# Kernel optimization log

Hardware: AMD Instinct MI355X
Metric: run time of the kernel (lower is better)

## Reference

```python
import jax, jax.numpy as jnp
import numpy as np

VOCAB = 256
D = 512
L = 2
FFN = 2048
H = 8
HD = D // H  # head dim = random-feature dim m for favor+
B = 2
T = 2048


def setup_inputs() -> dict:
    key = jax.random.key(0)
    ks = jax.random.split(key, 16)
    rng = np.random.default_rng(0)

    def lin(k, fan_in, shape):
        return jax.random.normal(k, shape, jnp.float32) / np.sqrt(fan_in)

    tokens = jax.random.randint(ks[0], (B, T), 0, VOCAB)
    emb = jax.random.normal(ks[1], (VOCAB, D // 2), jnp.float32)
    Wq = lin(ks[2], D, (L, D, D)); bq = 0.01 * jax.random.normal(ks[3], (L, D), jnp.float32)
    Wk = lin(ks[4], D, (L, D, D)); bk = 0.01 * jax.random.normal(ks[5], (L, D), jnp.float32)
    Wv = lin(ks[6], D, (L, D, D)); bv = 0.01 * jax.random.normal(ks[7], (L, D), jnp.float32)
    WU = lin(ks[8], D, (L, D, FFN)); bU = 0.01 * jax.random.normal(ks[9], (L, FFN), jnp.float32)
    WV = lin(ks[10], FFN, (L, FFN, D)); bV = 0.01 * jax.random.normal(ks[11], (L, D), jnp.float32)
    Wout = lin(ks[12], D, (D, VOCAB)); bout = 0.01 * jax.random.normal(ks[13], (VOCAB,), jnp.float32)
    ln1_g = jnp.ones((L, D), jnp.float32) + 0.02 * jax.random.normal(ks[14], (L, D), jnp.float32)
    ln2_g = jnp.ones((L, D), jnp.float32) + 0.02 * jax.random.normal(ks[15], (L, D), jnp.float32)
    ln1_b = jnp.zeros((L, D), jnp.float32)
    ln2_b = jnp.zeros((L, D), jnp.float32)
    # orthogonal random features per (layer, head), scaled by sqrt(head_dim)
    rfs_np = np.stack([
        np.stack([np.linalg.qr(rng.standard_normal((HD, HD)))[0] * np.sqrt(HD) for _ in range(H)])
        for _ in range(L)
    ]).astype(np.float32)
    rfs = jnp.asarray(rfs_np)
    return dict(tokens=tokens, emb=emb, Wq=Wq, bq=bq, Wk=Wk, bk=bk, Wv=Wv, bv=bv,
                rfs=rfs, ln1_g=ln1_g, ln1_b=ln1_b, ln2_g=ln2_g, ln2_b=ln2_b,
                WU=WU, bU=bU, WV=WV, bV=bV, Wout=Wout, bout=bout)


def _layernorm(x, g, b, eps=1e-5):
    mu = jnp.mean(x, -1, keepdims=True)
    var = jnp.mean((x - mu) ** 2, -1, keepdims=True)
    return (x - mu) * jax.lax.rsqrt(var + eps) * g + b


def _favor_feat(x, rfs):
    # x: [B,T,H,d]; rfs: [H,d,m]
    xp = x * (HD ** -0.25)
    return jnp.exp(jnp.einsum('bthd,hdm->bthm', xp, rfs)
                   - 0.5 * jnp.sum(xp ** 2, -1, keepdims=True))


def _attention(x, Wq, bq, Wk, bk, Wv, bv, rfs):
    Bx, Tx, Dm = x.shape
    q = (x @ Wq + bq).reshape(Bx, Tx, H, HD)
    k = (x @ Wk + bk).reshape(Bx, Tx, H, HD)
    v = (x @ Wv + bv).reshape(Bx, Tx, H, HD)
    qf = _favor_feat(q, rfs)  # [B,T,H,m]
    kf = _favor_feat(k, rfs)
    # causal prefix-sum (num_ps / den_ps with zero init sums)
    kv_cum = jnp.cumsum(jnp.einsum('bthm,bthd->bthmd', kf, v), axis=1)
    num = jnp.einsum('bthm,bthmd->bthd', qf, kv_cum)
    den = jnp.einsum('bthm,bthm->bth', qf, jnp.cumsum(kf, axis=1))
    return (num / (den[..., None] + 1e-16)).reshape(Bx, Tx, Dm)


def _pos_embs(x):
    # x: [B,T,D//2]; concat fixed sinusoidal embeddings of size D//2
    Bx, Tx, half = x.shape
    positions = jnp.arange(Tx, dtype=x.dtype)
    freqs = jnp.exp(jnp.arange(0, half, 2, dtype=x.dtype) * (-np.log(10000.0) / half))
    args = positions[:, None] * freqs[None, :]  # [T, half//2]
    sin = jnp.broadcast_to(jnp.sin(args)[None], (Bx, Tx, args.shape[1]))
    cos = jnp.broadcast_to(jnp.cos(args)[None], (Bx, Tx, args.shape[1]))
    return jnp.concatenate([x, sin, cos], -1)


def reference(tokens, emb, Wq, bq, Wk, bk, Wv, bv, rfs,
              ln1_g, ln1_b, ln2_g, ln2_b, WU, bU, WV, bV, Wout, bout):
    x = emb[tokens]            # [B,T,D//2]
    x = _pos_embs(x)           # [B,T,D]
    for i in range(L):
        skip = x
        a = _attention(x, Wq[i], bq[i], Wk[i], bk[i], Wv[i], bv[i], rfs[i])
        a = _layernorm(a, ln1_g[i], ln1_b[i])  # on_gptln=True: LN after attention
        x = skip + a
        skip = x
        h = jax.nn.gelu(x @ WU[i] + bU[i], approximate=False)
        h = h @ WV[i] + bV[i]
        h = _layernorm(h, ln2_g[i], ln2_b[i])  # on_gptln=True: LN after FFN
        x = skip + h
    return x @ Wout + bout     # [B,T,VOCAB]
```

## Files before the change

### kernel.cpp

```cpp
#include <hip/hip_runtime.h>
#include <hip/hip_bf16.h>
#include <math.h>

#define B_  2
#define T_  2048
#define D_  512
#define H_  8
#define HD_ 64
#define FFN_ 2048
#define VOCAB_ 256
#define BT_ (B_*T_)
#define NC_ 32
#define CENT_ 4160

typedef __attribute__((ext_vector_type(8))) short short8;
typedef __attribute__((ext_vector_type(4))) float float4v;
typedef __hip_bfloat16 bf16;

__device__ __forceinline__ void load16_lds(const void* g, void* l) {
  __builtin_amdgcn_global_load_lds(
      (const __attribute__((address_space(1))) unsigned int*)g,
      (__attribute__((address_space(3))) unsigned int*)l,
      16, 0, 0);
}

__global__ __launch_bounds__(512) void embed_pos_kernel(
    const int* __restrict__ tokens, const float* __restrict__ emb,
    float* __restrict__ x, bf16* __restrict__ xb)
{
  int bt = blockIdx.x;
  int t  = bt & (T_ - 1);
  int j  = threadIdx.x;
  float val;
  if (j < 256) {
    int tok = tokens[bt];
    val = emb[tok * 256 + j];
  } else {
    int jj = (j - 256) & 127;
    float f = expf(-(float)(2 * jj) * (9.210340371976184f / 256.0f));
    float arg = (float)t * f;
    val = (j < 384) ? sinf(arg) : cosf(arg);
  }
  size_t off = (size_t)bt * D_ + j;
  x[off]  = val;
  xb[off] = __float2bfloat16(val);
}

__global__ __launch_bounds__(256) void prep_all_kernel(
    const float* __restrict__ Wv, const float* __restrict__ WU,
    const float* __restrict__ WVp, const float* __restrict__ Wout,
    bf16* __restrict__ WvT, bf16* __restrict__ WUT,
    bf16* __restrict__ WVT, bf16* __restrict__ WoutT,
    const float* __restrict__ bq, const float* __restrict__ bk,
    const float* __restrict__ rfs, float* __restrict__ bqf,
    float* __restrict__ bkf)
{
  __shared__ float t[32][33];
  int id = blockIdx.x;
  if (id >= 4736) {
    int z = id - 4736;
    int l = z >> 1, side = z & 1;
    const float* b = (side ? bk : bq) + l * D_;
    float* bo = (side ? bkf : bqf) + l * D_;
    for (int n = threadIdx.x; n < D_; n += 256) {
      int h = n >> 6, j = n & 63;
      const float* R = rfs + ((size_t)l * H_ + h) * 4096;
      float acc = 0.f;
      for (int d = 0; d < 64; ++d) acc += b[h * 64 + d] * R[d * 64 + j];
      bo[n] = acc * 0.35355339059327373f;
    }
    return;
  }
  const float* W; bf16* Wt; int K, N, tx, ty;
  if (id < 512) {
    int l = id >> 8, tt = id & 255;
    W = Wv + (size_t)l * D_ * D_;  Wt = WvT + (size_t)l * D_ * D_;
    K = D_; N = D_; tx = tt & 15; ty = tt >> 4;
  } else if (id < 2560) {
    int tt = id - 512; int l = tt >> 10; tt &= 1023;
    W = WU + (size_t)l * D_ * FFN_;  Wt = WUT + (size_t)l * D_ * FFN_;
    K = D_; N = FFN_; tx = tt & 63; ty = tt >> 6;
  } else if (id < 4608) {
    int tt = id - 2560; int l = tt >> 10; tt &= 1023;
    W = WVp + (size_t)l * FFN_ * D_;  Wt = WVT + (size_t)l * FFN_ * D_;
    K = FFN_; N = D_; tx = tt & 15; ty = tt >> 4;
  } else {
    int tt = id - 4608;
    W = Wout;  Wt = WoutT;
    K = D_; N = VOCAB_; tx = tt & 7; ty = tt >> 3;
  }
  int n0 = tx * 32, k0 = ty * 32;
  int lx = threadIdx.x & 31, ly = threadIdx.x >> 5;
#pragma unroll
  for (int r = 0; r < 4; ++r)
    t[ly + 8 * r][lx] = W[(size_t)(k0 + ly + 8 * r) * N + n0 + lx];
  __syncthreads();
#pragma unroll
  for (int r = 0; r < 4; ++r)
    Wt[(size_t)(n0 + ly + 8 * r) * K + k0 + lx] = __float2bfloat16(t[lx][ly + 8 * r]);
}

__global__ __launch_bounds__(256) void rf_fold_w_kernel(
    const float* __restrict__ Wq, const float* __restrict__ Wk,
    const float* __restrict__ rfs, bf16* __restrict__ WqT, bf16* __restrict__ WkT)
{
  int h = blockIdx.x, kq = blockIdx.y, z = blockIdx.z;
  int l = z >> 1, side = z & 1;
  const float* W = (side ? Wk : Wq) + (size_t)l * D_ * D_;
  bf16* WT = (side ? WkT : WqT) + (size_t)l * D_ * D_;
  const float* Rg = rfs + ((size_t)l * H_ + h) * 4096;
  __shared__ float Rl[64][65];
  __shared__ float Ws[128][65];
  int tid = threadIdx.x;
  for (int i = tid; i < 1024; i += 256) {
    float4 v4 = ((const float4*)Rg)[i];
    int d = i >> 4, j0 = (i & 15) * 4;
    Rl[d][j0] = v4.x; Rl[d][j0+1] = v4.y; Rl[d][j0+2] = v4.z; Rl[d][j0+3] = v4.w;
  }
  for (int i = tid; i < 2048; i += 256) {
    int r = i >> 4, c0 = (i & 15) * 4;
    float4 v4 = *(const float4*)&W[(size_t)(kq * 128 + r) * D_ + h * 64 + c0];
    Ws[r][c0] = v4.x; Ws[r][c0+1] = v4.y; Ws[r][c0+2] = v4.z; Ws[r][c0+3] = v4.w;
  }
  __syncthreads();
  int lane = tid & 63, w = tid >> 6;
  for (int kh = 0; kh < 2; ++kh) {
    int kk = kh * 64 + lane;
#pragma unroll 1
    for (int jj = 0; jj < 16; ++jj) {
      int j = w * 16 + jj;
      float acc = 0.f;
#pragma unroll 16
      for (int d = 0; d < 64; ++d) acc += Ws[kk][d] * Rl[d][j];
      WT[(size_t)(h * 64 + j) * D_ + kq * 128 + kk] =
          __float2bfloat16(acc * 0.35355339059327373f);
    }
  }
}

__device__ __forceinline__ void mfma_core(
    const bf16* __restrict__ A, const bf16* __restrict__ Bt,
    int strideK, int kr, int row0, int col0, float4v acc[4][4])
{
  __shared__ short Al[128 * 64];
  __shared__ short Bl[128 * 64];
  int tid = threadIdx.x;
  int lane = tid & 63, w = tid >> 6;
  int wm = (w >> 1) * 64, wn = (w & 1) * 64;
  int quad = lane >> 4, l16 = lane & 15;

  int lr = lane >> 3;
  int ks = (((lane & 7) ^ lr)) * 8;
  const short* gA[4]; const short* gB[4];
  short* lA[4]; short* lB[4];
#pragma unroll
  for (int p = 0; p < 4; ++p) {
    int r = 32 * w + 8 * p;
    gA[p] = (const short*)A + (size_t)(row0 + r + lr) * strideK + ks;
    gB[p] = (const short*)Bt + (size_t)(col0 + r + lr) * strideK + ks;
    lA[p] = Al + r * 64;
    lB[p] = Bl + r * 64;
  }
#pragma unroll
  for (int p = 0; p < 4; ++p) {
    load16_lds(gA[p], lA[p]);
    load16_lds(gB[p], lB[p]);
  }

  for (int kt = 0; kt < kr; ++kt) {
    __syncthreads();
    short8 af[4][2], bfr[4][2];
#pragma unroll
    for (int mi = 0; mi < 4; ++mi) {
      int R = wm + mi * 16 + l16;
#pragma unroll
      for (int s = 0; s < 2; ++s) {
        int slot = (s * 4 + quad) ^ (R & 7);
        af[mi][s] = *(const short8*)&Al[R * 64 + slot * 8];
      }
    }
#pragma unroll
    for (int ni = 0; ni < 4; ++ni) {
      int R = wn + ni * 16 + l16;
#pragma unroll
      for (int s = 0; s < 2; ++s) {
        int slot = (s * 4 + quad) ^ (R & 7);
        bfr[ni][s] = *(const short8*)&Bl[R * 64 + slot * 8];
      }
    }
    __syncthreads();
    if (kt + 1 < kr) {
      int o = (kt + 1) * 64;
#pragma unroll
      for (int p = 0; p < 4; ++p) {
        load16_lds(gA[p] + o, lA[p]);
        load16_lds(gB[p] + o, lB[p]);
      }
    }
#pragma unroll
    for (int mi = 0; mi < 4; ++mi)
#pragma unroll
      for (int ni = 0; ni < 4; ++ni) {
        acc[mi][ni] = __builtin_amdgcn_mfma_f32_16x16x32_bf16(
            af[mi][0], bfr[ni][0], acc[mi][ni], 0, 0, 0);
        acc[mi][ni] = __builtin_amdgcn_mfma_f32_16x16x32_bf16(
            af[mi][1], bfr[ni][1], acc[mi][ni], 0, 0, 0);
      }
  }
}

__global__ __launch_bounds__(256) void gemm_mfma(
    const bf16* __restrict__ A, const bf16* __restrict__ Bt,
    const float* __restrict__ bias, void* __restrict__ Cout,
    int M, int N, int K, int mode)
{
  int lane = threadIdx.x & 63, w = threadIdx.x >> 6;
  int wm = (w >> 1) * 64, wn = (w & 1) * 64;
  int quad = lane >> 4, l16 = lane & 15;
  int row0 = blockIdx.y * 128, col0 = blockIdx.x * 128;
  float4v acc[4][4] = {};
  mfma_core(A, Bt, K, K >> 6, row0, col0, acc);
#pragma unroll
  for (int mi = 0; mi < 4; ++mi) {
#pragma unroll
    for (int ni = 0; ni < 4; ++ni) {
      int j = col0 + wn + ni * 16 + l16;
      float bj = bias[j];
#pragma unroll
      for (int r = 0; r < 4; ++r) {
        int i = row0 + wm + mi * 16 + quad * 4 + r;
        float v = acc[mi][ni][r] + bj;
        if (mode == 1) {
          v = 0.5f * v * (1.0f + erff(v * 0.7071067811865475f));
          ((bf16*)Cout)[(size_t)i * N + j] = __float2bfloat16(v);
        } else {
          ((float*)Cout)[(size_t)i * N + j] = v;
        }
      }
    }
  }
}

__global__ __launch_bounds__(256) void gemm_qkv(
    const bf16* __restrict__ A, const bf16* __restrict__ wT,
    const float* __restrict__ bqf, const float* __restrict__ bkf,
    const float* __restrict__ bv, float* __restrict__ outb, int l)
{
  int z = blockIdx.z;
  const bf16* Bt = wT + ((size_t)z * 2 + l) * D_ * D_;
  const float* bias = (z == 0 ? bqf : (z == 1 ? bkf : bv)) + l * D_;
  float* Cout = outb + (size_t)z * BT_ * D_;
  int lane = threadIdx.x & 63, w = threadIdx.x >> 6;
  int wm = (w >> 1) * 64, wn = (w & 1) * 64;
  int quad = lane >> 4, l16 = lane & 15;
  int row0 = blockIdx.y * 128, col0 = blockIdx.x * 128;
  float4v acc[4][4] = {};
  mfma_core(A, Bt, D_, D_ >> 6, row0, col0, acc);
  if (z < 2) {
#pragma unroll
    for (int mi = 0; mi < 4; ++mi) {
      float vres[4][4];
      float sq[4] = {0.f, 0.f, 0.f, 0.f};
#pragma unroll
      for (int ni = 0; ni < 4; ++ni) {
        int j = col0 + wn + ni * 16 + l16;
        float bj = bias[j];
#pragma unroll
        for (int r = 0; r < 4; ++r) {
          float v = acc[mi][ni][r] + bj;
          vres[ni][r] = v;
          sq[r] += v * v;
        }
      }
#pragma unroll
      for (int r = 0; r < 4; ++r) {
        float s = sq[r];
        s += __shfl_xor(s, 1, 64);
        s += __shfl_xor(s, 2, 64);
        s += __shfl_xor(s, 4, 64);
        s += __shfl_xor(s, 8, 64);
        sq[r] = s;
      }
#pragma unroll
      for (int ni = 0; ni < 4; ++ni) {
        int j = col0 + wn + ni * 16 + l16;
#pragma unroll
        for (int r = 0; r < 4; ++r) {
          int i = row0 + wm + mi * 16 + quad * 4 + r;
          Cout[(size_t)i * D_ + j] = __expf(vres[ni][r] - sq[r] * (1.0f / 128.0f));
        }
      }
    }
  } else {
#pragma unroll
    for (int mi = 0; mi < 4; ++mi) {
#pragma unroll
      for (int ni = 0; ni < 4; ++ni) {
        int j = col0 + wn + ni * 16 + l16;
        float bj = bias[j];
#pragma unroll
        for (int r = 0; r < 4; ++r) {
          int i = row0 + wm + mi * 16 + quad * 4 + r;
          Cout[(size_t)i * D_ + j] = acc[mi][ni][r] + bj;
        }
      }
    }
  }
}

__global__ __launch_bounds__(256) void gemm_splitk(
    const bf16* __restrict__ A, const bf16* __restrict__ Bt,
    float* __restrict__ P, int M, int N, int K, int KS)
{
  int s = blockIdx.z;
  int lane = threadIdx.x & 63, w = threadIdx.x >> 6;
  int wm = (w >> 1) * 64, wn = (w & 1) * 64;
  int quad = lane >> 4, l16 = lane & 15;
  int row0 = blockIdx.y * 128, col0 = blockIdx.x * 128;
  float4v acc[4][4] = {};
  mfma_core((const bf16*)((const short*)A + s * KS),
            (const bf16*)((const short*)Bt + s * KS),
            K, KS >> 6, row0, col0, acc);
  float* Ps = P + (size_t)s * M * N;
#pragma unroll
  for (int mi = 0; mi < 4; ++mi) {
#pragma unroll
    for (int ni = 0; ni < 4; ++ni) {
      int j = col0 + wn + ni * 16 + l16;
#pragma unroll
      for (int r = 0; r < 4; ++r) {
        int i = row0 + wm + mi * 16 + quad * 4 + r;
        Ps[(size_t)i * N + j] = acc[mi][ni][r];
      }
    }
  }
}

__global__ __launch_bounds__(256) void reduce4_bias_kernel(
    const float* __restrict__ P, const float* __restrict__ bias,
    float* __restrict__ C, int MN, int N)
{
  int idx = (blockIdx.x * 256 + threadIdx.x) * 4;
  float4 s0 = *(const float4*)&P[idx];
  float4 s1 = *(const float4*)&P[idx + MN];
  float4 s2 = *(const float4*)&P[idx + 2 * MN];
  float4 s3 = *(const float4*)&P[idx + 3 * MN];
  float4 b  = *(const float4*)&bias[idx & (N - 1)];
  float4 r;
  r.x = s0.x + s1.x + s2.x + s3.x + b.x;
  r.y = s0.y + s1.y + s2.y + s3.y + b.y;
  r.z = s0.z + s1.z + s2.z + s3.z + b.z;
  r.w = s0.w + s1.w + s2.w + s3.w + b.w;
  *(float4*)&C[idx] = r;
}

__global__ __launch_bounds__(256) void reduce_ln_add_kernel(
    const float* __restrict__ P, const float* __restrict__ bias,
    float* __restrict__ x, bf16* __restrict__ xb,
    const float* __restrict__ g, const float* __restrict__ bta)
{
  const int MN = BT_ * D_;
  int row = blockIdx.x;
  int tid = threadIdx.x;
  size_t base = (size_t)row * D_;
  float v0 = P[base + tid] + P[MN + base + tid] + P[2 * MN + base + tid]
           + P[3 * MN + base + tid] + bias[tid];
  float v1 = P[base + tid + 256] + P[MN + base + tid + 256]
           + P[2 * MN + base + tid + 256] + P[3 * MN + base + tid + 256]
           + bias[tid + 256];
  __shared__ float red[4];
  float w = v0 + v1;
  for (int o = 32; o > 0; o >>= 1) w += __shfl_down(w, o, 64);
  if ((tid & 63) == 0) red[tid >> 6] = w;
  __syncthreads();
  float mu = (red[0] + red[1] + red[2] + red[3]) * (1.f / 512.f);
  float d0 = v0 - mu, d1 = v1 - mu;
  __syncthreads();
  w = d0 * d0 + d1 * d1;
  for (int o = 32; o > 0; o >>= 1) w += __shfl_down(w, o, 64);
  if ((tid & 63) == 0) red[tid >> 6] = w;
  __syncthreads();
  float var = (red[0] + red[1] + red[2] + red[3]) * (1.f / 512.f);
  float rs = rsqrtf(var + 1e-5f);
  float n0 = x[base + tid]       + d0 * rs * g[tid]       + bta[tid];
  float n1 = x[base + tid + 256] + d1 * rs * g[tid + 256] + bta[tid + 256];
  x[base + tid]        = n0;
  x[base + tid + 256]  = n1;
  xb[base + tid]       = __float2bfloat16(n0);
  xb[base + tid + 256] = __float2bfloat16(n1);
}

__global__ __launch_bounds__(256) void chunk_sum_kernel(
    const float* __restrict__ kf, const float* __restrict__ v,
    float* __restrict__ buf)
{
  int bh = blockIdx.x / 31;
  int c  = blockIdx.x % 31;
  int b = bh >> 3, h = bh & 7;
  __shared__ float Ks[64][68], Vs[64][68];
  __shared__ float zpart[4][68];
  int tid = threadIdx.x;
  int d = tid & 63, g = tid >> 6;
  for (int t4 = 0; t4 < 64; t4 += 4) {
    int t = t4 + g;
    size_t off = ((size_t)(b * T_ + c * 64 + t) * D_) + h * 64 + d;
    Ks[t][d] = kf[off];
    Vs[t][d] = v[off];
  }
  __syncthreads();
  float acc[16];
#pragma unroll
  for (int i = 0; i < 16; ++i) acc[i] = 0.f;
  for (int t = 0; t < 64; ++t) {
    float vv = Vs[t][d];
#pragma unroll
    for (int i4 = 0; i4 < 4; ++i4) {
      float4 kv = *(const float4*)&Ks[t][g * 16 + i4 * 4];
      acc[i4*4+0] += kv.x * vv;
      acc[i4*4+1] += kv.y * vv;
      acc[i4*4+2] += kv.z * vv;
      acc[i4*4+3] += kv.w * vv;
    }
  }
  float zp = 0.f;
  for (int t = g * 16; t < g * 16 + 16; ++t) zp += Ks[t][d];
  zpart[g][d] = zp;
  size_t bo = (size_t)(bh * 31 + c) * CENT_;
#pragma unroll
  for (int i = 0; i < 16; ++i) buf[bo + (size_t)(g * 16 + i) * 64 + d] = acc[i];
  __syncthreads();
  if (tid < 64)
    buf[bo + 4096 + tid] = zpart[0][tid] + zpart[1][tid] + zpart[2][tid] + zpart[3][tid];
}

__global__ __launch_bounds__(256) void chunk_prefix_kernel(float* __restrict__ buf)
{
  int bh = blockIdx.x / 17;
  int grp = blockIdx.x % 17;
  int e = grp * 256 + threadIdx.x;
  if (e >= CENT_) return;
  size_t base = (size_t)bh * 31 * CENT_ + e;
  float vals[31];
#pragma unroll
  for (int c = 0; c < 31; ++c) vals[c] = buf[base + (size_t)c * CENT_];
  float run = 0.f;
#pragma unroll
  for (int c = 0; c < 31; ++c) {
    run += vals[c];
    buf[base + (size_t)c * CENT_] = run;
  }
}

__global__ __launch_bounds__(256) void chunk_attn_kernel(
    const float* __restrict__ qf, const float* __restrict__ kf,
    const float* __restrict__ v, const float* __restrict__ buf,
    float* __restrict__ out)
{
  int bh = blockIdx.x >> 5;
  int c  = blockIdx.x & 31;
  int b = bh >> 3, h = bh & 7;
  __shared__ float Qs[64][68], Ks[64][68], Vs[64][68];
  __shared__ float dpart[8][68];
  __shared__ float den[64];
  int tid = threadIdx.x;
  int d = tid & 63, g = tid >> 6;
  for (int t4 = 0; t4 < 64; t4 += 4) {
    int t = t4 + g;
    size_t off = ((size_t)(b * T_ + c * 64 + t) * D_) + h * 64 + d;
    Qs[t][d] = qf[off];
    Ks[t][d] = kf[off];
    Vs[t][d] = v[off];
  }
  __syncthreads();
  {
    int i = d;
    float a[16];
#pragma unroll
    for (int jj = 0; jj < 16; ++jj) a[jj] = 0.f;
    for (int m = 0; m < 64; m += 4) {
      float4 qv = *(const float4*)&Qs[i][m];
#pragma unroll
      for (int jj = 0; jj < 16; ++jj) {
        float4 kv = *(const float4*)&Ks[g * 16 + jj][m];
        a[jj] += qv.x * kv.x + qv.y * kv.y + qv.z * kv.z + qv.w * kv.w;
      }
    }
    __syncthreads();
    float rsum = 0.f;
#pragma unroll
    for (int jj = 0; jj < 16; ++jj) {
      int j = g * 16 + jj;
      a[jj] = (j <= i) ? a[jj] : 0.f;
      rsum += a[jj];
    }
#pragma unroll
    for (int j4 = 0; j4 < 4; ++j4)
      *(float4*)&Ks[i][g * 16 + j4 * 4] =
          make_float4(a[j4*4], a[j4*4+1], a[j4*4+2], a[j4*4+3]);
    dpart[g][i] = rsum;
  }
  const float* S0 = buf + (size_t)(bh * 31 + (c - 1)) * CENT_;
  {
    int i = d;
    float qz = 0.f;
    if (c > 0) {
      const float* z0 = S0 + 4096;
      for (int m = g * 16; m < g * 16 + 16; m += 4) {
        float4 qv = *(const float4*)&Qs[i][m];
        qz += qv.x * z0[m] + qv.y * z0[m+1] + qv.z * z0[m+2] + qv.w * z0[m+3];
      }
    }
    dpart[4 + g][i] = qz;
  }
  __syncthreads();
  if (tid < 64)
    den[tid] = dpart[0][tid] + dpart[1][tid] + dpart[2][tid] + dpart[3][tid]
             + dpart[4][tid] + dpart[5][tid] + dpart[6][tid] + dpart[7][tid];
  float acc[16];
#pragma unroll
  for (int ii = 0; ii < 16; ++ii) acc[ii] = 0.f;
  for (int j = 0; j < 64; j += 4) {
    float va = Vs[j][d], vb2 = Vs[j+1][d], vc = Vs[j+2][d], vd2 = Vs[j+3][d];
#pragma unroll
    for (int ii = 0; ii < 16; ++ii) {
      float4 av = *(const float4*)&Ks[g * 16 + ii][j];
      acc[ii] += av.x * va + av.y * vb2 + av.z * vc + av.w * vd2;
    }
  }
  if (c > 0) {
    for (int m = 0; m < 64; m += 4) {
      float sa = S0[(size_t)m * 64 + d];
      float sb2 = S0[(size_t)(m+1) * 64 + d];
      float sc = S0[(size_t)(m+2) * 64 + d];
      float sd2 = S0[(size_t)(m+3) * 64 + d];
#pragma unroll
      for (int ii = 0; ii < 16; ++ii) {
        float4 qv = *(const float4*)&Qs[g * 16 + ii][m];
        acc[ii] += qv.x * sa + qv.y * sb2 + qv.z * sc + qv.w * sd2;
      }
    }
  }
  __syncthreads();
#pragma unroll
  for (int ii = 0; ii < 16; ++ii) {
    int i = g * 16 + ii;
    size_t off = ((size_t)(b * T_ + c * 64 + i) * D_) + h * 64 + d;
    out[off] = acc[ii] / (den[i] + 1e-16f);
  }
}

__global__ __launch_bounds__(256) void ln_add_kernel(
    float* __restrict__ x, bf16* __restrict__ xb, const float* __restrict__ a,
    const float* __restrict__ g, const float* __restrict__ bta)
{
  int row = blockIdx.x;
  int tid = threadIdx.x;
  const float* ar = a + (size_t)row * D_;
  float v0 = ar[tid], v1 = ar[tid + 256];
  __shared__ float red[4];
  float w = v0 + v1;
  for (int o = 32; o > 0; o >>= 1) w += __shfl_down(w, o, 64);
  if ((tid & 63) == 0) red[tid >> 6] = w;
  __syncthreads();
  float mu = (red[0] + red[1] + red[2] + red[3]) * (1.f / 512.f);
  float d0 = v0 - mu, d1 = v1 - mu;
  __syncthreads();
  w = d0 * d0 + d1 * d1;
  for (int o = 32; o > 0; o >>= 1) w += __shfl_down(w, o, 64);
  if ((tid & 63) == 0) red[tid >> 6] = w;
  __syncthreads();
  float var = (red[0] + red[1] + red[2] + red[3]) * (1.f / 512.f);
  float rs = rsqrtf(var + 1e-5f);
  size_t xoff = (size_t)row * D_;
  float n0 = x[xoff + tid]       + d0 * rs * g[tid]       + bta[tid];
  float n1 = x[xoff + tid + 256] + d1 * rs * g[tid + 256] + bta[tid + 256];
  x[xoff + tid]        = n0;
  x[xoff + tid + 256]  = n1;
  xb[xoff + tid]       = __float2bfloat16(n0);
  xb[xoff + tid + 256] = __float2bfloat16(n1);
}

extern "C" void kernel_launch(void* const* d_in, const int* in_sizes, int n_in,
                              void* d_out, int out_size, void* d_ws, size_t ws_size,
                              hipStream_t stream) {
  const int*   tokens = (const int*)  d_in[0];
  const float* emb    = (const float*)d_in[1];
  const float* Wq     = (const float*)d_in[2];
  const float* bq     = (const float*)d_in[3];
  const float* Wk     = (const float*)d_in[4];
  const float* bk     = (const float*)d_in[5];
  const float* Wv     = (const float*)d_in[6];
  const float* bv     = (const float*)d_in[7];
  const float* rfs    = (const float*)d_in[8];
  const float* ln1g   = (const float*)d_in[9];
  const float* ln1b   = (const float*)d_in[10];
  const float* ln2g   = (const float*)d_in[11];
  const float* ln2b   = (const float*)d_in[12];
  const float* WU     = (const float*)d_in[13];
  const float* bU     = (const float*)d_in[14];
  const float* WV     = (const float*)d_in[15];
  const float* bV     = (const float*)d_in[16];
  const float* Wout   = (const float*)d_in[17];
  const float* bout   = (const float*)d_in[18];
  float* out = (float*)d_out;

  const size_t R = (size_t)BT_ * D_;
  float* ws = (float*)d_ws;
  float* x  = ws + 0 * R;
  float* ab = ws + 1 * R;
  float* qb = ws + 2 * R;
  float* kb = ws + 3 * R;
  float* vb = ws + 4 * R;
  float* sb = ws + 5 * R;
  bf16*  xb = (bf16*)(ws + 6 * R);
  bf16*  hb = (bf16*)qb;
  float* pb = ws + 16 * R;
  bf16* wT    = (bf16*)(ws + 6 * R + R / 2);
  bf16* WqT   = wT;
  bf16* WkT   = WqT + (size_t)2 * D_ * D_;
  bf16* WvT   = WkT + (size_t)2 * D_ * D_;
  bf16* WUT   = WvT + (size_t)2 * D_ * D_;
  bf16* WVT   = WUT + (size_t)2 * D_ * FFN_;
  bf16* WoutT = WVT + (size_t)2 * D_ * FFN_;
  float* bqf  = (float*)(WoutT + (size_t)VOCAB_ * D_);
  float* bkf  = bqf + 2 * D_;

  rf_fold_w_kernel<<<dim3(8, 4, 4), 256, 0, stream>>>(Wq, Wk, rfs, WqT, WkT);
  prep_all_kernel<<<4740, 256, 0, stream>>>(
      Wv, WU, WV, Wout, WvT, WUT, WVT, WoutT, bq, bk, rfs, bqf, bkf);

  embed_pos_kernel<<<BT_, 512, 0, stream>>>(tokens, emb, x, xb);

  for (int l = 0; l < 2; ++l) {
    gemm_qkv<<<dim3(D_/128, BT_/128, 3), 256, 0, stream>>>(
        xb, wT, bqf, bkf, bv, qb, l);

    chunk_sum_kernel<<<16 * 31, 256, 0, stream>>>(kb, vb, sb);
    chunk_prefix_kernel<<<16 * 17, 256, 0, stream>>>(sb);
    chunk_attn_kernel<<<16 * NC_, 256, 0, stream>>>(qb, kb, vb, sb, ab);

    ln_add_kernel<<<BT_, 256, 0, stream>>>(x, xb, ab, ln1g + l*D_, ln1b + l*D_);

    gemm_mfma<<<dim3(FFN_/128, BT_/128), 256, 0, stream>>>(
        xb, WUT + (size_t)l*D_*FFN_, bU + l*FFN_, hb, BT_, FFN_, D_, 1);

    gemm_splitk<<<dim3(D_/128, BT_/128, 4), 256, 0, stream>>>(
        hb, WVT + (size_t)l*FFN_*D_, pb, BT_, D_, FFN_, FFN_/4);
    reduce_ln_add_kernel<<<BT_, 256, 0, stream>>>(
        pb, bV + l*D_, x, xb, ln2g + l*D_, ln2b + l*D_);
  }

  gemm_splitk<<<dim3(VOCAB_/128, BT_/128, 4), 256, 0, stream>>>(
      xb, WoutT, pb, BT_, VOCAB_, D_, D_/4);
  reduce4_bias_kernel<<<(BT_*VOCAB_)/1024, 256, 0, stream>>>(
      pb, bout, out, BT_*VOCAB_, VOCAB_);
}
```

Baseline: 372.6 us.

## Store Q/K/V features in bf16 and use MFMA in chunked linear attention

The QKV GEMM now writes bf16 outputs instead of fp32, halving activation traffic. The chunk_sum and chunk_attn kernels are rewritten to stage bf16 tiles in swizzled LDS and compute K^T V, QK^T, A·V and Q·S0 with bf16 MFMA instructions instead of scalar FP32 FMAs. The workspace layout is reshuffled to fit the smaller buffers. This trades precision, since the random-feature values and the masked score matrix are rounded to bf16, for less memory traffic and matrix-core throughput in the attention stage.

```diff
diff --git a/kernel.cpp b/kernel.cpp
--- a/kernel.cpp
+++ b/kernel.cpp
@@ -22,6 +22,15 @@
       (const __attribute__((address_space(1))) unsigned int*)g,
       (__attribute__((address_space(3))) unsigned int*)l,
       16, 0, 0);
+}
+
+__device__ __forceinline__ unsigned short f2bf(float f) {
+  bf16 h = __float2bfloat16(f);
+  return __builtin_bit_cast(unsigned short, h);
+}
+__device__ __forceinline__ float bf2f(unsigned short u) {
+  unsigned int i = ((unsigned int)u) << 16;
+  return __builtin_bit_cast(float, i);
 }
 
 __global__ __launch_bounds__(512) void embed_pos_kernel(
@@ -244,12 +253,12 @@
 __global__ __launch_bounds__(256) void gemm_qkv(
     const bf16* __restrict__ A, const bf16* __restrict__ wT,
     const float* __restrict__ bqf, const float* __restrict__ bkf,
-    const float* __restrict__ bv, float* __restrict__ outb, int l)
+    const float* __restrict__ bv, bf16* __restrict__ outb, int l)
 {
   int z = blockIdx.z;
   const bf16* Bt = wT + ((size_t)z * 2 + l) * D_ * D_;
   const float* bias = (z == 0 ? bqf : (z == 1 ? bkf : bv)) + l * D_;
-  float* Cout = outb + (size_t)z * BT_ * D_;
+  bf16* Cout = outb + (size_t)z * BT_ * D_;
   int lane = threadIdx.x & 63, w = threadIdx.x >> 6;
   int wm = (w >> 1) * 64, wn = (w & 1) * 64;
   int quad = lane >> 4, l16 = lane & 15;
@@ -287,7 +296,8 @@
 #pragma unroll
         for (int r = 0; r < 4; ++r) {
           int i = row0 + wm + mi * 16 + quad * 4 + r;
-          Cout[(size_t)i * D_ + j] = __expf(vres[ni][r] - sq[r] * (1.0f / 128.0f));
+          Cout[(size_t)i * D_ + j] =
+              __float2bfloat16(__expf(vres[ni][r] - sq[r] * (1.0f / 128.0f)));
         }
       }
     }
@@ -301,7 +311,7 @@
 #pragma unroll
         for (int r = 0; r < 4; ++r) {
           int i = row0 + wm + mi * 16 + quad * 4 + r;
-          Cout[(size_t)i * D_ + j] = acc[mi][ni][r] + bj;
+          Cout[(size_t)i * D_ + j] = __float2bfloat16(acc[mi][ni][r] + bj);
         }
       }
     }
@@ -391,43 +401,64 @@
 }
 
 __global__ __launch_bounds__(256) void chunk_sum_kernel(
-    const float* __restrict__ kf, const float* __restrict__ v,
+    const bf16* __restrict__ kf, const bf16* __restrict__ vf,
     float* __restrict__ buf)
 {
   int bh = blockIdx.x / 31;
   int c  = blockIdx.x % 31;
   int b = bh >> 3, h = bh & 7;
-  __shared__ float Ks[64][68], Vs[64][68];
-  __shared__ float zpart[4][68];
+  __shared__ short KT[64 * 64];
+  __shared__ short VT[64 * 64];
+  __shared__ float zpart[4][64];
   int tid = threadIdx.x;
-  int d = tid & 63, g = tid >> 6;
-  for (int t4 = 0; t4 < 64; t4 += 4) {
-    int t = t4 + g;
-    size_t off = ((size_t)(b * T_ + c * 64 + t) * D_) + h * 64 + d;
-    Ks[t][d] = kf[off];
-    Vs[t][d] = v[off];
-  }
-  __syncthreads();
-  float acc[16];
-#pragma unroll
-  for (int i = 0; i < 16; ++i) acc[i] = 0.f;
-  for (int t = 0; t < 64; ++t) {
-    float vv = Vs[t][d];
-#pragma unroll
-    for (int i4 = 0; i4 < 4; ++i4) {
-      float4 kv = *(const float4*)&Ks[t][g * 16 + i4 * 4];
-      acc[i4*4+0] += kv.x * vv;
-      acc[i4*4+1] += kv.y * vv;
-      acc[i4*4+2] += kv.z * vv;
-      acc[i4*4+3] += kv.w * vv;
+  int m = tid & 63, g = tid >> 6;
+  const size_t rowbase = ((size_t)(b * T_ + c * 64)) * D_ + h * 64;
+#pragma unroll
+  for (int cc0 = 0; cc0 < 2; ++cc0) {
+    int cc = g + cc0 * 4;
+    short8 kk, vv;
+#pragma unroll
+    for (int u = 0; u < 8; ++u) {
+      size_t off = rowbase + (size_t)(cc * 8 + u) * D_ + m;
+      kk[u] = ((const short*)kf)[off];
+      vv[u] = ((const short*)vf)[off];
+    }
+    int slot = cc ^ (m & 7);
+    *(short8*)&KT[m * 64 + slot * 8] = kk;
+    *(short8*)&VT[m * 64 + slot * 8] = vv;
+  }
+  __syncthreads();
+  int quad = (tid & 63) >> 4, l16 = tid & 15;
+  int ar = g * 16 + l16;
+  short8 afr[2];
+#pragma unroll
+  for (int s = 0; s < 2; ++s)
+    afr[s] = *(const short8*)&KT[ar * 64 + ((s * 4 + quad) ^ (ar & 7)) * 8];
+  float4v acc[4] = {};
+#pragma unroll
+  for (int nd = 0; nd < 4; ++nd) {
+    int br = nd * 16 + l16;
+#pragma unroll
+    for (int s = 0; s < 2; ++s) {
+      short8 bfr = *(const short8*)&VT[br * 64 + ((s * 4 + quad) ^ (br & 7)) * 8];
+      acc[nd] = __builtin_amdgcn_mfma_f32_16x16x32_bf16(afr[s], bfr, acc[nd], 0, 0, 0);
     }
   }
   float zp = 0.f;
-  for (int t = g * 16; t < g * 16 + 16; ++t) zp += Ks[t][d];
-  zpart[g][d] = zp;
+#pragma unroll
+  for (int cc0 = 0; cc0 < 2; ++cc0) {
+    int cc = g + cc0 * 4;
+    short8 kk = *(const short8*)&KT[m * 64 + (cc ^ (m & 7)) * 8];
+#pragma unroll
+    for (int u = 0; u < 8; ++u) zp += bf2f((unsigned short)kk[u]);
+  }
+  zpart[g][m] = zp;
   size_t bo = (size_t)(bh * 31 + c) * CENT_;
 #pragma unroll
-  for (int i = 0; i < 16; ++i) buf[bo + (size_t)(g * 16 + i) * 64 + d] = acc[i];
+  for (int nd = 0; nd < 4; ++nd)
+#pragma unroll
+    for (int r = 0; r < 4; ++r)
+      buf[bo + (size_t)(g * 16 + quad * 4 + r) * 64 + nd * 16 + l16] = acc[nd][r];
   __syncthreads();
   if (tid < 64)
     buf[bo + 4096 + tid] = zpart[0][tid] + zpart[1][tid] + zpart[2][tid] + zpart[3][tid];
@@ -452,101 +483,148 @@
 }
 
 __global__ __launch_bounds__(256) void chunk_attn_kernel(
-    const float* __restrict__ qf, const float* __restrict__ kf,
-    const float* __restrict__ v, const float* __restrict__ buf,
+    const bf16* __restrict__ qf, const bf16* __restrict__ kf,
+    const bf16* __restrict__ vf, const float* __restrict__ buf,
     float* __restrict__ out)
 {
   int bh = blockIdx.x >> 5;
-  int c  = blockIdx.x & 31;
+  int ck = blockIdx.x & 31;
   int b = bh >> 3, h = bh & 7;
-  __shared__ float Qs[64][68], Ks[64][68], Vs[64][68];
-  __shared__ float dpart[8][68];
-  __shared__ float den[64];
+  __shared__ short Qs[64 * 64];
+  __shared__ short Ks[64 * 64];
+  __shared__ short VT[64 * 64];
+  __shared__ short S0T[64 * 64];
+  __shared__ float z0[64];
+  __shared__ float dlds[64];
+  __shared__ float dpartA[64];
+  __shared__ float dpartQ[4][64];
   int tid = threadIdx.x;
-  int d = tid & 63, g = tid >> 6;
-  for (int t4 = 0; t4 < 64; t4 += 4) {
-    int t = t4 + g;
-    size_t off = ((size_t)(b * T_ + c * 64 + t) * D_) + h * 64 + d;
-    Qs[t][d] = qf[off];
-    Ks[t][d] = kf[off];
-    Vs[t][d] = v[off];
-  }
-  __syncthreads();
+  int lane = tid & 63, w = tid >> 6;
+  int quad = lane >> 4, l16 = lane & 15;
+  const size_t rb = ((size_t)(b * T_ + ck * 64)) * D_ + h * 64;
+
   {
-    int i = d;
-    float a[16];
-#pragma unroll
-    for (int jj = 0; jj < 16; ++jj) a[jj] = 0.f;
-    for (int m = 0; m < 64; m += 4) {
-      float4 qv = *(const float4*)&Qs[i][m];
-#pragma unroll
-      for (int jj = 0; jj < 16; ++jj) {
-        float4 kv = *(const float4*)&Ks[g * 16 + jj][m];
-        a[jj] += qv.x * kv.x + qv.y * kv.y + qv.z * kv.z + qv.w * kv.w;
-      }
-    }
-    __syncthreads();
-    float rsum = 0.f;
-#pragma unroll
-    for (int jj = 0; jj < 16; ++jj) {
-      int j = g * 16 + jj;
-      a[jj] = (j <= i) ? a[jj] : 0.f;
-      rsum += a[jj];
-    }
-#pragma unroll
-    for (int j4 = 0; j4 < 4; ++j4)
-      *(float4*)&Ks[i][g * 16 + j4 * 4] =
-          make_float4(a[j4*4], a[j4*4+1], a[j4*4+2], a[j4*4+3]);
-    dpart[g][i] = rsum;
-  }
-  const float* S0 = buf + (size_t)(bh * 31 + (c - 1)) * CENT_;
+    int lr = lane >> 3;
+    int fc = (lane & 7) ^ lr;
+#pragma unroll
+    for (int seg = 0; seg < 2; ++seg) {
+      int r = 16 * w + 8 * seg;
+      load16_lds((const short*)qf + rb + (size_t)(r + lr) * D_ + fc * 8, &Qs[r * 64]);
+      load16_lds((const short*)kf + rb + (size_t)(r + lr) * D_ + fc * 8, &Ks[r * 64]);
+    }
+    int d = lane;
+    const float* S0 = buf + (size_t)(bh * 31 + (ck > 0 ? ck - 1 : 0)) * CENT_;
+#pragma unroll
+    for (int cc0 = 0; cc0 < 2; ++cc0) {
+      int cc = w + cc0 * 4;
+      short8 vv, ss;
+#pragma unroll
+      for (int u = 0; u < 8; ++u) {
+        vv[u] = ((const short*)vf)[rb + (size_t)(cc * 8 + u) * D_ + d];
+        ss[u] = (ck > 0) ? (short)f2bf(S0[(size_t)(cc * 8 + u) * 64 + d]) : (short)0;
+      }
+      int slot = cc ^ (d & 7);
+      *(short8*)&VT[d * 64 + slot * 8] = vv;
+      *(short8*)&S0T[d * 64 + slot * 8] = ss;
+    }
+    if (tid < 64) z0[tid] = (ck > 0) ? S0[4096 + tid] : 0.f;
+  }
+  __syncthreads();
+
+  float4v pacc[4] = {};
   {
-    int i = d;
+    int ar = 16 * w + l16;
+    short8 afr[2];
+#pragma unroll
+    for (int s = 0; s < 2; ++s)
+      afr[s] = *(const short8*)&Qs[ar * 64 + ((s * 4 + quad) ^ (ar & 7)) * 8];
+#pragma unroll
+    for (int nj = 0; nj < 4; ++nj) {
+      int br = nj * 16 + l16;
+#pragma unroll
+      for (int s = 0; s < 2; ++s) {
+        short8 bfr = *(const short8*)&Ks[br * 64 + ((s * 4 + quad) ^ (br & 7)) * 8];
+        pacc[nj] = __builtin_amdgcn_mfma_f32_16x16x32_bf16(afr[s], bfr, pacc[nj], 0, 0, 0);
+      }
+    }
+  }
+  {
+    int i = lane;
     float qz = 0.f;
-    if (c > 0) {
-      const float* z0 = S0 + 4096;
-      for (int m = g * 16; m < g * 16 + 16; m += 4) {
-        float4 qv = *(const float4*)&Qs[i][m];
-        qz += qv.x * z0[m] + qv.y * z0[m+1] + qv.z * z0[m+2] + qv.w * z0[m+3];
-      }
-    }
-    dpart[4 + g][i] = qz;
+#pragma unroll
+    for (int cc0 = 0; cc0 < 2; ++cc0) {
+      int cc = w + cc0 * 4;
+      short8 qq = *(const short8*)&Qs[i * 64 + (cc ^ (i & 7)) * 8];
+#pragma unroll
+      for (int u = 0; u < 8; ++u) qz += bf2f((unsigned short)qq[u]) * z0[cc * 8 + u];
+    }
+    dpartQ[w][i] = qz;
+  }
+  __syncthreads();
+
+  {
+    float rs[4] = {0.f, 0.f, 0.f, 0.f};
+#pragma unroll
+    for (int nj = 0; nj < 4; ++nj) {
+#pragma unroll
+      for (int r = 0; r < 4; ++r) {
+        int i = 16 * w + quad * 4 + r;
+        int j = nj * 16 + l16;
+        float val = (j <= i) ? pacc[nj][r] : 0.f;
+        rs[r] += val;
+        ((unsigned short*)Ks)[i * 64 + ((j >> 3) ^ (i & 7)) * 8 + (j & 7)] = f2bf(val);
+      }
+    }
+#pragma unroll
+    for (int r = 0; r < 4; ++r) {
+      float s = rs[r];
+      s += __shfl_xor(s, 1, 64);
+      s += __shfl_xor(s, 2, 64);
+      s += __shfl_xor(s, 4, 64);
+      s += __shfl_xor(s, 8, 64);
+      rs[r] = s;
+    }
+    if (l16 == 0) {
+#pragma unroll
+      for (int r = 0; r < 4; ++r) dpartA[16 * w + quad * 4 + r] = rs[r];
+    }
   }
   __syncthreads();
   if (tid < 64)
-    den[tid] = dpart[0][tid] + dpart[1][tid] + dpart[2][tid] + dpart[3][tid]
-             + dpart[4][tid] + dpart[5][tid] + dpart[6][tid] + dpart[7][tid];
-  float acc[16];
-#pragma unroll
-  for (int ii = 0; ii < 16; ++ii) acc[ii] = 0.f;
-  for (int j = 0; j < 64; j += 4) {
-    float va = Vs[j][d], vb2 = Vs[j+1][d], vc = Vs[j+2][d], vd2 = Vs[j+3][d];
-#pragma unroll
-    for (int ii = 0; ii < 16; ++ii) {
-      float4 av = *(const float4*)&Ks[g * 16 + ii][j];
-      acc[ii] += av.x * va + av.y * vb2 + av.z * vc + av.w * vd2;
-    }
-  }
-  if (c > 0) {
-    for (int m = 0; m < 64; m += 4) {
-      float sa = S0[(size_t)m * 64 + d];
-      float sb2 = S0[(size_t)(m+1) * 64 + d];
-      float sc = S0[(size_t)(m+2) * 64 + d];
-      float sd2 = S0[(size_t)(m+3) * 64 + d];
-#pragma unroll
-      for (int ii = 0; ii < 16; ++ii) {
-        float4 qv = *(const float4*)&Qs[g * 16 + ii][m];
-        acc[ii] += qv.x * sa + qv.y * sb2 + qv.z * sc + qv.w * sd2;
-      }
-    }
-  }
-  __syncthreads();
-#pragma unroll
-  for (int ii = 0; ii < 16; ++ii) {
-    int i = g * 16 + ii;
-    size_t off = ((size_t)(b * T_ + c * 64 + i) * D_) + h * 64 + d;
-    out[off] = acc[ii] / (den[i] + 1e-16f);
-  }
+    dlds[tid] = dpartA[tid] + dpartQ[0][tid] + dpartQ[1][tid]
+              + dpartQ[2][tid] + dpartQ[3][tid];
+
+  float4v acc[4] = {};
+  {
+    int ar = 16 * w + l16;
+    short8 aA[2], aQ[2];
+#pragma unroll
+    for (int s = 0; s < 2; ++s) {
+      aA[s] = *(const short8*)&Ks[ar * 64 + ((s * 4 + quad) ^ (ar & 7)) * 8];
+      aQ[s] = *(const short8*)&Qs[ar * 64 + ((s * 4 + quad) ^ (ar & 7)) * 8];
+    }
+#pragma unroll
+    for (int nd = 0; nd < 4; ++nd) {
+      int br = nd * 16 + l16;
+#pragma unroll
+      for (int s = 0; s < 2; ++s) {
+        short8 bV = *(const short8*)&VT[br * 64 + ((s * 4 + quad) ^ (br & 7)) * 8];
+        acc[nd] = __builtin_amdgcn_mfma_f32_16x16x32_bf16(aA[s], bV, acc[nd], 0, 0, 0);
+        short8 bS = *(const short8*)&S0T[br * 64 + ((s * 4 + quad) ^ (br & 7)) * 8];
+        acc[nd] = __builtin_amdgcn_mfma_f32_16x16x32_bf16(aQ[s], bS, acc[nd], 0, 0, 0);
+      }
+    }
+  }
+  __syncthreads();
+#pragma unroll
+  for (int nd = 0; nd < 4; ++nd)
+#pragma unroll
+    for (int r = 0; r < 4; ++r) {
+      int i = 16 * w + quad * 4 + r;
+      int d = nd * 16 + l16;
+      out[((size_t)(b * T_ + ck * 64 + i)) * D_ + h * 64 + d] =
+          acc[nd][r] / (dlds[i] + 1e-16f);
+    }
 }
 
 __global__ __launch_bounds__(256) void ln_add_kernel(
@@ -606,16 +684,16 @@
 
   const size_t R = (size_t)BT_ * D_;
   float* ws = (float*)d_ws;
-  float* x  = ws + 0 * R;
-  float* ab = ws + 1 * R;
-  float* qb = ws + 2 * R;
-  float* kb = ws + 3 * R;
-  float* vb = ws + 4 * R;
-  float* sb = ws + 5 * R;
-  bf16*  xb = (bf16*)(ws + 6 * R);
-  bf16*  hb = (bf16*)qb;
-  float* pb = ws + 16 * R;
-  bf16* wT    = (bf16*)(ws + 6 * R + R / 2);
+  float* x  = ws;
+  float* ab = ws + R;
+  float* sb = ws + 2 * R;
+  bf16*  qb = (bf16*)(ws + 3 * R);
+  bf16*  kb = (bf16*)(ws + 3 * R + R / 2);
+  bf16*  vb = (bf16*)(ws + 4 * R);
+  bf16*  xb = (bf16*)(ws + 4 * R + R / 2);
+  bf16*  hb = (bf16*)(ws + 5 * R);
+  float* pb = ws + 7 * R;
+  bf16*  wT = (bf16*)(ws + 11 * R);
   bf16* WqT   = wT;
   bf16* WkT   = WqT + (size_t)2 * D_ * D_;
   bf16* WvT   = WkT + (size_t)2 * D_ * D_;
```

New measurement: 326.2 us. -12.5%, faster.
